# Kernel tuning notes

Measured on AMD Instinct MI355X. Metric: run time of the kernel, lower is better.

## Reference

```python
import jax, jax.numpy as jnp
import numpy as np

K = 20
EPS = 1e-5


def knn_idx(x, k):
    # x: (B,C,N); returns indices of k nearest neighbors (largest negative sq dist)
    xx = jnp.sum(x * x, axis=1)                       # (B,N)
    inner = jnp.einsum('bcn,bcm->bnm', x, x)          # (B,N,N)
    dist = 2.0 * inner - xx[:, :, None] - xx[:, None, :]
    return jax.lax.top_k(dist, k)[1]                  # (B,N,k)


def gather_nb(x, idx):
    # x: (B,C,N), idx: (B,N,k) -> (B,N,k,C)
    xt = jnp.transpose(x, (0, 2, 1))
    return jax.vmap(lambda t, i: t[i])(xt, idx)


def bn(x, g, b, m, v):
    # eval-mode batchnorm over channel axis 1
    sh = [1] * x.ndim
    sh[1] = -1
    inv = g / jnp.sqrt(v + EPS)
    return (x - m.reshape(sh)) * inv.reshape(sh) + b.reshape(sh)


def graph_feature(x, k=K):
    # x: (B,C,N) -> (B,3C,N,k): [neighbor, center, center-neighbor]
    idx = knn_idx(x, k)
    nb = gather_nb(x, idx)                            # (B,N,k,C)
    ctr = jnp.broadcast_to(jnp.transpose(x, (0, 2, 1))[:, :, None, :], nb.shape)
    f = jnp.concatenate([nb, ctr, ctr - nb], axis=-1)
    return jnp.transpose(f, (0, 3, 1, 2))


def att_pool(x, g, b, m, v, W, wb):
    # x: (B,C,N,k); BN->ReLU->1x1 conv -> softmax over k -> weighted sum
    h = jax.nn.relu(bn(x, g, b, m, v))
    act = jnp.einsum('bcnk,oc->bonk', h, W) + wb[None, :, None, None]
    scores = jax.nn.softmax(act, axis=-1)
    return jnp.sum(x * scores, axis=-1)               # (B,C,N)


def lafe(x, W1, b1, W2, b2, W3, b3):
    # local attention extraction; x: (B,3,N) -> (B,16,N)
    idx = knn_idx(x, K)
    nb = gather_nb(x, idx)                            # (B,N,k,3)
    ctr = jnp.broadcast_to(jnp.transpose(x, (0, 2, 1))[:, :, None, :], nb.shape)
    x_n = ctr - nb
    new_f = jnp.einsum('bnkc,oc->bnko', ctr, W1) + b1
    self_att = jnp.einsum('bnko,o->bnk', new_f, W3[0]) + b3[0]
    edge = jnp.einsum('bnkc,oc->bnko', x_n, W2) + b2  # (B,N,k,16)
    nb_att = jnp.einsum('bnko,o->bnk', edge, W3[0]) + b3[0]
    logits = self_att + nb_att                        # (B,N,k)
    coefs = jax.nn.softmax(jax.nn.leaky_relu(logits, 0.01), axis=-1)
    vals = jnp.einsum('bnk,bnko->bno', coefs, edge)   # (B,N,16)
    return jnp.transpose(jax.nn.elu(vals), (0, 2, 1))


def _forward(x, law1, lab1, law2, lab2, law3, lab3,
             mlp_w, mlp_b, mlp_g, mlp_be, mlp_m, mlp_v,
             c1_w, bn1_g, bn1_b, bn1_m, bn1_v,
             p1_g, p1_b, p1_m, p1_v, p1_w, p1_wb,
             c2_w, bn2_g, bn2_b, bn2_m, bn2_v,
             p2_g, p2_b, p2_m, p2_v, p2_w, p2_wb,
             c3_w, bn3_g, bn3_b, bn3_m, bn3_v):
    xm = lafe(x, law1, lab1, law2, lab2, law3, lab3)          # (B,16,N)
    x_manet = jnp.concatenate([x, xm], axis=1)                # (B,19,N)
    x_mlp = jax.nn.relu(bn(jnp.einsum('bcn,oc->bon', x_manet, mlp_w) + mlp_b[None, :, None],
                           mlp_g, mlp_be, mlp_m, mlp_v))      # (B,256,N)
    g = graph_feature(x_manet)                                # (B,57,N,k)
    h1 = jax.nn.leaky_relu(bn(jnp.einsum('bcnk,oc->bonk', g, c1_w),
                              bn1_g, bn1_b, bn1_m, bn1_v), 0.2)
    x_p1 = att_pool(h1, p1_g, p1_b, p1_m, p1_v, p1_w, p1_wb)  # (B,64,N)
    x_c1 = jnp.concatenate([x_manet, x_p1], axis=1)           # (B,83,N)
    g2 = graph_feature(x_c1)                                  # (B,249,N,k)
    h2 = jax.nn.leaky_relu(bn(jnp.einsum('bcnk,oc->bonk', g2, c2_w),
                              bn2_g, bn2_b, bn2_m, bn2_v), 0.2)
    x_p2 = att_pool(h2, p2_g, p2_b, p2_m, p2_v, p2_w, p2_wb)  # (B,256,N)
    x_c2 = jnp.concatenate([x_mlp, x_p2], axis=1)             # (B,512,N)
    return jax.nn.leaky_relu(bn(jnp.einsum('bcn,oc->bon', x_c2, c3_w),
                                bn3_g, bn3_b, bn3_m, bn3_v), 0.2)


def setup_inputs() -> dict:
    key = jax.random.key(0)
    ks = iter(jax.random.split(key, 16))
    f32 = jnp.float32
    def W(*s):
        return jax.random.normal(next(ks), s, f32) * 0.05
    B, N = 8, 2048
    def bn_params(c):
        return jnp.ones((c,), f32), jnp.zeros((c,), f32), jnp.zeros((c,), f32), jnp.ones((c,), f32)
    d = {}
    d['x'] = jax.random.normal(next(ks), (B, 3, N), f32)
    d['law1'], d['lab1'] = W(16, 3), jnp.zeros((16,), f32)
    d['law2'], d['lab2'] = W(16, 3), jnp.zeros((16,), f32)
    d['law3'], d['lab3'] = W(1, 16), jnp.zeros((1,), f32)
    d['mlp_w'], d['mlp_b'] = W(256, 19), jnp.zeros((256,), f32)
    d['mlp_g'], d['mlp_be'], d['mlp_m'], d['mlp_v'] = bn_params(256)
    d['c1_w'] = W(64, 57)
    d['bn1_g'], d['bn1_b'], d['bn1_m'], d['bn1_v'] = bn_params(64)
    d['p1_g'], d['p1_b'], d['p1_m'], d['p1_v'] = bn_params(64)
    d['p1_w'], d['p1_wb'] = W(64, 64), jnp.zeros((64,), f32)
    d['c2_w'] = W(256, 249)
    d['bn2_g'], d['bn2_b'], d['bn2_m'], d['bn2_v'] = bn_params(256)
    d['p2_g'], d['p2_b'], d['p2_m'], d['p2_v'] = bn_params(256)
    d['p2_w'], d['p2_wb'] = W(256, 256), jnp.zeros((256,), f32)
    d['c3_w'] = W(512, 512)
    d['bn3_g'], d['bn3_b'], d['bn3_m'], d['bn3_v'] = bn_params(512)
    return d


def reference(x, law1, lab1, law2, lab2, law3, lab3,
              mlp_w, mlp_b, mlp_g, mlp_be, mlp_m, mlp_v,
              c1_w, bn1_g, bn1_b, bn1_m, bn1_v,
              p1_g, p1_b, p1_m, p1_v, p1_w, p1_wb,
              c2_w, bn2_g, bn2_b, bn2_m, bn2_v,
              p2_g, p2_b, p2_m, p2_v, p2_w, p2_wb,
              c3_w, bn3_g, bn3_b, bn3_m, bn3_v):
    return _forward(x, law1, lab1, law2, lab2, law3, lab3,
                    mlp_w, mlp_b, mlp_g, mlp_be, mlp_m, mlp_v,
                    c1_w, bn1_g, bn1_b, bn1_m, bn1_v,
                    p1_g, p1_b, p1_m, p1_v, p1_w, p1_wb,
                    c2_w, bn2_g, bn2_b, bn2_m, bn2_v,
                    p2_g, p2_b, p2_m, p2_v, p2_w, p2_wb,
                    c3_w, bn3_g, bn3_b, bn3_m, bn3_v)
```

## Files before the change

kernel.cpp:

```cpp
#include <hip/hip_runtime.h>
#include <math.h>
#include <float.h>

#define NB 8
#define NP 2048
#define KNN 20
#define BN_EPS 1e-5f

typedef __attribute__((ext_vector_type(8))) short short8v;
typedef __attribute__((ext_vector_type(4))) float f32x4;
typedef __attribute__((ext_vector_type(16))) float f32x16;

__device__ __forceinline__ float leakyf(float x, float s) { return x >= 0.f ? x : s * x; }

__device__ __forceinline__ unsigned short f2bf(float f) {
  unsigned u = __float_as_uint(f);
  u = u + 0x7fffu + ((u >> 16) & 1u);
  return (unsigned short)(u >> 16);
}
__device__ __forceinline__ float bf2f(unsigned short h) {
  return __uint_as_float((unsigned)h << 16);
}
__device__ __forceinline__ unsigned sortkey(float f) {
  unsigned u = __float_as_uint(f);
  return (u & 0x80000000u) ? ~u : (u | 0x80000000u);
}

__global__ void transpose_k(const float* __restrict__ src, float* __restrict__ dst, int O, int C) {
  int i = blockIdx.x * 256 + threadIdx.x;
  if (i < O * C) { int o = i / C, c = i - o * C; dst[c * O + o] = src[i]; }
}

__global__ void copy_ch_k(const float* __restrict__ src, int srcC,
                          float* __restrict__ dst, int dstC, int row0, int nch) {
  int i = blockIdx.x * 256 + threadIdx.x;
  int total = NB * nch * NP;
  if (i < total) {
    int n = i & (NP - 1); int t = i >> 11; int c = t % nch; int b = t / nch;
    dst[((size_t)b * dstC + row0 + c) * NP + n] = src[((size_t)b * srcC + c) * NP + n];
  }
}

__global__ void xx_k(const float* __restrict__ src, int C, float* __restrict__ xx) {
  int i = blockIdx.x * 256 + threadIdx.x;
  if (i < NB * NP) {
    int n = i & (NP - 1); int b = i >> 11;
    const float* xb = src + (size_t)b * C * NP + n;
    float s = 0.f;
    for (int c = 0; c < C; ++c) { float v = xb[(size_t)c * NP]; s += v * v; }
    xx[i] = s;
  }
}

#define DKC 16
__global__ __launch_bounds__(256) void dist_k(const float* __restrict__ src, int C,
                                              const float* __restrict__ xx,
                                              float* __restrict__ D, int b0) {
  __shared__ float sA[DKC][64];
  __shared__ float sB[DKC][64];
  int bz = blockIdx.z; int b = b0 + bz;
  int n0 = blockIdx.x * 64, m0 = blockIdx.y * 64;
  int tid = threadIdx.x;
  int tn = tid >> 4, tm = tid & 15;
  float acc[4][4] = {};
  const float* xb = src + (size_t)b * C * NP;
  for (int k0 = 0; k0 < C; k0 += DKC) {
    for (int t = tid; t < DKC * 64; t += 256) {
      int kk = t >> 6, i = t & 63;
      int c = k0 + kk;
      float a = 0.f, bb = 0.f;
      if (c < C) { a = xb[(size_t)c * NP + n0 + i]; bb = xb[(size_t)c * NP + m0 + i]; }
      sA[kk][i] = a; sB[kk][i] = bb;
    }
    __syncthreads();
#pragma unroll
    for (int kk = 0; kk < DKC; ++kk) {
      float av[4], bv[4];
#pragma unroll
      for (int q = 0; q < 4; ++q) { av[q] = sA[kk][tn * 4 + q]; bv[q] = sB[kk][tm * 4 + q]; }
#pragma unroll
      for (int qi = 0; qi < 4; ++qi)
#pragma unroll
        for (int qj = 0; qj < 4; ++qj) acc[qi][qj] += av[qi] * bv[qj];
    }
    __syncthreads();
  }
  const float* xxb = xx + (size_t)b * NP;
#pragma unroll
  for (int qi = 0; qi < 4; ++qi) {
    int n = n0 + tn * 4 + qi; float xn = xxb[n];
#pragma unroll
    for (int qj = 0; qj < 4; ++qj) {
      int m = m0 + tm * 4 + qj;
      D[((size_t)bz * NP + n) * NP + m] = 2.f * acc[qi][qj] - xn - xxb[m];
    }
  }
}

__global__ __launch_bounds__(64) void topk_k(const float* __restrict__ D,
                                             int* __restrict__ idxo, int rowbase) {
  int row = blockIdx.x;
  const float* d = D + (size_t)row * NP;
  int lane = threadIdx.x;
  float v[32];
#pragma unroll
  for (int j = 0; j < 32; ++j) v[j] = d[lane + 64 * j];
  int* out = idxo + (size_t)(rowbase + row) * KNN;
  for (int it = 0; it < KNN; ++it) {
    float bv = v[0]; int bj = 0;
#pragma unroll
    for (int j = 1; j < 32; ++j) { if (v[j] > bv) { bv = v[j]; bj = j; } }
    int bm = lane + 64 * bj;
    unsigned long long key = ((unsigned long long)sortkey(bv) << 32) | (unsigned)(~bm);
#pragma unroll
    for (int off = 1; off < 64; off <<= 1) {
      unsigned long long ok = __shfl_xor(key, off);
      if (ok > key) key = ok;
    }
    int bmw = ~(unsigned)key;
    if (lane == 0) out[it] = bmw;
    if ((bmw & 63) == lane) v[bmw >> 6] = -FLT_MAX;
  }
}

__global__ __launch_bounds__(64) void lafe_k(const float* __restrict__ x, const int* __restrict__ idx,
                                             const float* __restrict__ W1, const float* __restrict__ b1,
                                             const float* __restrict__ W2, const float* __restrict__ b2,
                                             const float* __restrict__ W3, const float* __restrict__ b3,
                                             float* __restrict__ x_manet) {
  int t = blockIdx.x * 64 + threadIdx.x;
  if (t >= NB * NP) return;
  int b = t >> 11, n = t & (NP - 1);
  const float* xb = x + (size_t)b * 3 * NP;
  float ctr[3];
#pragma unroll
  for (int c = 0; c < 3; ++c) ctr[c] = xb[c * NP + n];
  float self_s = b3[0];
#pragma unroll
  for (int o = 0; o < 16; ++o) {
    float nf = b1[o];
#pragma unroll
    for (int c = 0; c < 3; ++c) nf += ctr[c] * W1[o * 3 + c];
    self_s += nf * W3[o];
  }
  const int* id = idx + (size_t)t * KNN;
  float logit[KNN];
  float mx = -FLT_MAX;
  for (int k = 0; k < KNN; ++k) {
    int j = id[k];
    float xn[3];
#pragma unroll
    for (int c = 0; c < 3; ++c) xn[c] = ctr[c] - xb[c * NP + j];
    float natt = b3[0];
#pragma unroll
    for (int o = 0; o < 16; ++o) {
      float e = b2[o];
#pragma unroll
      for (int c = 0; c < 3; ++c) e += xn[c] * W2[o * 3 + c];
      natt += e * W3[o];
    }
    float lg = self_s + natt;
    lg = leakyf(lg, 0.01f);
    logit[k] = lg; mx = fmaxf(mx, lg);
  }
  float s = 0.f;
#pragma unroll
  for (int k = 0; k < KNN; ++k) { logit[k] = expf(logit[k] - mx); s += logit[k]; }
  float invs = 1.f / s;
  float vals[16] = {};
  for (int k = 0; k < KNN; ++k) {
    int j = id[k];
    float xn[3];
#pragma unroll
    for (int c = 0; c < 3; ++c) xn[c] = ctr[c] - xb[c * NP + j];
    float w = logit[k] * invs;
#pragma unroll
    for (int o = 0; o < 16; ++o) {
      float e = b2[o];
#pragma unroll
      for (int c = 0; c < 3; ++c) e += xn[c] * W2[o * 3 + c];
      vals[o] += w * e;
    }
  }
#pragma unroll
  for (int o = 0; o < 16; ++o) {
    float v = vals[o];
    v = v > 0.f ? v : expm1f(v);
    x_manet[((size_t)b * 19 + 3 + o) * NP + n] = v;
  }
}

__global__ __launch_bounds__(256) void mlp_k(const float* __restrict__ xman, const float* __restrict__ wt,
                                             const float* __restrict__ bias,
                                             const float* __restrict__ g, const float* __restrict__ be,
                                             const float* __restrict__ m, const float* __restrict__ v,
                                             unsigned short* __restrict__ actT) {
  int o0 = (threadIdx.x & 31) * 8;
  int n = blockIdx.x * 8 + (threadIdx.x >> 5);
  int b = blockIdx.z;
  const float* xb = xman + (size_t)b * 19 * NP;
  float acc[8];
#pragma unroll
  for (int q = 0; q < 8; ++q) acc[q] = bias[o0 + q];
  for (int c = 0; c < 19; ++c) {
    float xv = xb[(size_t)c * NP + n];
    const float4* w4 = reinterpret_cast<const float4*>(wt + c * 256 + o0);
    float4 wa = w4[0], wb4 = w4[1];
    float wr[8] = {wa.x, wa.y, wa.z, wa.w, wb4.x, wb4.y, wb4.z, wb4.w};
#pragma unroll
    for (int q = 0; q < 8; ++q) acc[q] += xv * wr[q];
  }
  short8v hi8, lo8;
#pragma unroll
  for (int q = 0; q < 8; ++q) {
    int o = o0 + q;
    float inv = g[o] / sqrtf(v[o] + BN_EPS);
    float z = fmaxf((acc[q] - m[o]) * inv + be[o], 0.f);
    unsigned short h = f2bf(z);
    hi8[q] = (short)h;
    lo8[q] = (short)f2bf(z - bf2f(h));
  }
  size_t base = ((size_t)b * NP + n) * 1024;
  *reinterpret_cast<short8v*>(actT + base + o0) = hi8;
  *reinterpret_cast<short8v*>(actT + base + 512 + o0) = lo8;
}

__global__ __launch_bounds__(64, 1) void conv1pool_k(
    const float* __restrict__ xman, const int* __restrict__ idx,
    const float* __restrict__ c1wt,
    const float* __restrict__ b1g, const float* __restrict__ b1b,
    const float* __restrict__ b1m, const float* __restrict__ b1v,
    const float* __restrict__ p1g, const float* __restrict__ p1b,
    const float* __restrict__ p1m, const float* __restrict__ p1v,
    const float* __restrict__ p1wt, const float* __restrict__ p1wb,
    float* __restrict__ x_c1) {
  __shared__ __align__(16) float sg[64 * 20];
  __shared__ int jid[KNN];
  __shared__ float sctr[19];
  int t = blockIdx.x;
  int b = t >> 11, n = t & (NP - 1);
  int lane = threadIdx.x;
  const float* xb = xman + (size_t)b * 19 * NP;
  if (lane < KNN) jid[lane] = idx[(size_t)t * KNN + lane];
  else if (lane >= 32 && lane < 32 + 19) sctr[lane - 32] = xb[(size_t)(lane - 32) * NP + n];
  __syncthreads();
  for (int e = lane; e < 19 * KNN; e += 64) {
    int c = e / KNN, k = e - c * KNN;
    float ctrv = sctr[c];
    float nbv = xb[(size_t)c * NP + jid[k]];
    sg[c * 20 + k] = nbv;
    sg[(19 + c) * 20 + k] = ctrv;
    sg[(38 + c) * 20 + k] = ctrv - nbv;
  }
  __syncthreads();
  float h[KNN] = {};
  for (int c = 0; c < 57; ++c) {
    float wv = c1wt[c * 64 + lane];
    const float4* gp = reinterpret_cast<const float4*>(sg + c * 20);
    float4 A = gp[0], Bv = gp[1], Cv = gp[2], Dv = gp[3], E = gp[4];
    float gv[20] = {A.x,A.y,A.z,A.w,Bv.x,Bv.y,Bv.z,Bv.w,Cv.x,Cv.y,Cv.z,Cv.w,Dv.x,Dv.y,Dv.z,Dv.w,E.x,E.y,E.z,E.w};
#pragma unroll
    for (int k = 0; k < KNN; ++k) h[k] += wv * gv[k];
  }
  float inv1 = b1g[lane] / sqrtf(b1v[lane] + BN_EPS);
  float m1 = b1m[lane], bb1 = b1b[lane];
  float h1[KNN];
#pragma unroll
  for (int k = 0; k < KNN; ++k) {
    float z = (h[k] - m1) * inv1 + bb1;
    h1[k] = leakyf(z, 0.2f);
  }
  float pinv = p1g[lane] / sqrtf(p1v[lane] + BN_EPS);
  float pm = p1m[lane], pb = p1b[lane];
  __syncthreads();
#pragma unroll
  for (int k = 0; k < KNN; ++k) sg[lane * 20 + k] = fmaxf((h1[k] - pm) * pinv + pb, 0.f);
  __syncthreads();
  float act[KNN] = {};
  for (int c = 0; c < 64; ++c) {
    float wv = p1wt[c * 64 + lane];
    const float4* gp = reinterpret_cast<const float4*>(sg + c * 20);
    float4 A = gp[0], Bv = gp[1], Cv = gp[2], Dv = gp[3], E = gp[4];
    float gv[20] = {A.x,A.y,A.z,A.w,Bv.x,Bv.y,Bv.z,Bv.w,Cv.x,Cv.y,Cv.z,Cv.w,Dv.x,Dv.y,Dv.z,Dv.w,E.x,E.y,E.z,E.w};
#pragma unroll
    for (int k = 0; k < KNN; ++k) act[k] += wv * gv[k];
  }
  float wb = p1wb[lane];
  float mx = -FLT_MAX;
#pragma unroll
  for (int k = 0; k < KNN; ++k) { act[k] += wb; mx = fmaxf(mx, act[k]); }
  float s = 0.f, outv = 0.f;
#pragma unroll
  for (int k = 0; k < KNN; ++k) {
    float e = expf(act[k] - mx);
    s += e; outv += h1[k] * e;
  }
  x_c1[((size_t)b * 83 + 19 + lane) * NP + n] = outv / s;
}

__global__ void prep2_k(const float* __restrict__ c2w, unsigned short* __restrict__ Wnc) {
  int i = blockIdx.x * 256 + threadIdx.x;
  if (i >= 256 * 192) return;
  int o = i / 192, c = i - o * 192;
  unsigned short v = 0;
  if (c < 83) v = f2bf(c2w[o * 249 + c] - c2w[o * 249 + 166 + c]);
  else if (c >= 96 && c < 96 + 83) {
    int cc = c - 96;
    v = f2bf(c2w[o * 249 + 83 + cc] + c2w[o * 249 + 166 + cc]);
  }
  Wnc[o * 192 + c] = v;
}

__global__ void castbf_k(const float* __restrict__ src, unsigned short* __restrict__ dst, int n) {
  int i = blockIdx.x * 256 + threadIdx.x;
  if (i < n) dst[i] = f2bf(src[i]);
}

__global__ void packw_k(const unsigned short* __restrict__ Wsrc, int KS, int Kstride,
                        unsigned short* __restrict__ dst) {
  int i = blockIdx.x * 256 + threadIdx.x;
  if (i >= 8 * KS * 64) return;
  int lane = i & 63;
  int ks = (i >> 6) % KS;
  int ot = i / (64 * KS);
  int o = ot * 32 + (lane & 31);
  int c = ks * 16 + 8 * (lane >> 5);
#pragma unroll
  for (int e = 0; e < 8; ++e) dst[i * 8 + e] = Wsrc[(size_t)o * Kstride + c + e];
}

__global__ void prep3_k(const float* __restrict__ c3w, unsigned short* __restrict__ W3p) {
  int i = blockIdx.x * 256 + threadIdx.x;
  if (i >= 512 * 1024) return;
  int o = i >> 10, k = i & 1023;
  W3p[i] = f2bf(c3w[o * 512 + (k & 511)]);
}

__global__ void prepbn_k(const float* g2, const float* b2, const float* m2, const float* v2,
                         const float* pg, const float* pb, const float* pm, const float* pv,
                         float* __restrict__ fold) {
  int o = threadIdx.x;
  float s2 = g2[o] / sqrtf(v2[o] + BN_EPS);
  fold[o] = s2; fold[256 + o] = b2[o] - m2[o] * s2;
  float sp = pg[o] / sqrtf(pv[o] + BN_EPS);
  fold[512 + o] = sp; fold[768 + o] = pb[o] - pm[o] * sp;
}

__global__ void prepbn3_k(const float* g, const float* bb, const float* m, const float* v,
                          float* __restrict__ fold3) {
  int o = blockIdx.x * 256 + threadIdx.x;
  if (o < 512) {
    float s = g[o] / sqrtf(v[o] + BN_EPS);
    fold3[o] = s;
    fold3[512 + o] = bb[o] - m[o] * s;
  }
}

__global__ __launch_bounds__(256) void t2bf_k(const float* __restrict__ xc1,
                                              unsigned short* __restrict__ xc1T) {
  __shared__ unsigned short tile[256 * 96];
  int b = blockIdx.y;
  int n0 = blockIdx.x * 256;
  int tid = threadIdx.x;
  const float* xb = xc1 + (size_t)b * 83 * NP;
  for (int c = 0; c < 83; ++c)
    tile[tid * 96 + c] = f2bf(xb[(size_t)c * NP + n0 + tid]);
#pragma unroll
  for (int c = 83; c < 96; ++c) tile[tid * 96 + c] = 0;
  __syncthreads();
  const float4* src = (const float4*)tile;
  float4* dst = (float4*)(xc1T + ((size_t)b * NP + n0) * 96);
  for (int i = tid; i < 3072; i += 256) dst[i] = src[i];
}

__global__ __launch_bounds__(256, 2) void conv2mfma_k(
    const unsigned short* __restrict__ xc1T, const int* __restrict__ idx,
    const unsigned short* __restrict__ pw1, const unsigned short* __restrict__ pw2,
    const float* __restrict__ fold, unsigned short* __restrict__ actT) {
  __shared__ unsigned short nbF[2 * 6 * 64 * 8];
  __shared__ unsigned short hhF[2 * 16 * 64 * 8];
  __shared__ int jid[64];
  int tid = threadIdx.x;
  int t0 = blockIdx.x * 2;
  int b = t0 >> 11, n0 = t0 & (NP - 1);

  if (tid < 64) {
    int p = tid >> 5, kk = tid & 31;
    int kc = kk < KNN ? kk : KNN - 1;
    jid[tid] = idx[(size_t)(t0 + p) * KNN + kc];
  }
  __syncthreads();
  for (int it = tid; it < 768; it += 256) {
    int p = it >= 384; int rem = it - p * 384;
    int kk = rem / 12, seg = rem - kk * 12;
    int j = jid[p * 32 + kk];
    short8v v = *reinterpret_cast<const short8v*>(xc1T + ((size_t)b * NP + j) * 96 + seg * 8);
    int ks = seg >> 1, hi = seg & 1;
    *reinterpret_cast<short8v*>(&nbF[(((p * 6 + ks) << 6) + hi * 32 + kk) * 8]) = v;
  }
  __syncthreads();

  int w = tid >> 6, l = tid & 63;
  int kk = l & 31, hi = l >> 5;
  int ot0 = w * 2, ot1 = w * 2 + 1;
  const short8v* pw1v = (const short8v*)pw1;
  const short8v* pw2v = (const short8v*)pw2;

  f32x16 acc[2][2];
#pragma unroll
  for (int p = 0; p < 2; ++p)
#pragma unroll
    for (int nt = 0; nt < 2; ++nt)
#pragma unroll
      for (int r = 0; r < 16; ++r) acc[p][nt][r] = 0.f;

#pragma unroll
  for (int ks = 0; ks < 6; ++ks) {
    short8v b0 = pw1v[(ot0 * 12 + ks) * 64 + l];
    short8v b1 = pw1v[(ot1 * 12 + ks) * 64 + l];
    short8v a0 = *reinterpret_cast<const short8v*>(&nbF[((ks << 6) + l) * 8]);
    short8v a1 = *reinterpret_cast<const short8v*>(&nbF[(((6 + ks) << 6) + l) * 8]);
    acc[0][0] = __builtin_amdgcn_mfma_f32_32x32x16_bf16(a0, b0, acc[0][0], 0, 0, 0);
    acc[0][1] = __builtin_amdgcn_mfma_f32_32x32x16_bf16(a0, b1, acc[0][1], 0, 0, 0);
    acc[1][0] = __builtin_amdgcn_mfma_f32_32x32x16_bf16(a1, b0, acc[1][0], 0, 0, 0);
    acc[1][1] = __builtin_amdgcn_mfma_f32_32x32x16_bf16(a1, b1, acc[1][1], 0, 0, 0);
  }
  const unsigned short* ct0 = xc1T + ((size_t)b * NP + n0) * 96 + 8 * hi;
  const unsigned short* ct1 = ct0 + 96;
#pragma unroll
  for (int ks = 0; ks < 6; ++ks) {
    short8v b0 = pw1v[(ot0 * 12 + 6 + ks) * 64 + l];
    short8v b1 = pw1v[(ot1 * 12 + 6 + ks) * 64 + l];
    short8v a0 = *reinterpret_cast<const short8v*>(ct0 + ks * 16);
    short8v a1 = *reinterpret_cast<const short8v*>(ct1 + ks * 16);
    acc[0][0] = __builtin_amdgcn_mfma_f32_32x32x16_bf16(a0, b0, acc[0][0], 0, 0, 0);
    acc[0][1] = __builtin_amdgcn_mfma_f32_32x32x16_bf16(a0, b1, acc[0][1], 0, 0, 0);
    acc[1][0] = __builtin_amdgcn_mfma_f32_32x32x16_bf16(a1, b0, acc[1][0], 0, 0, 0);
    acc[1][1] = __builtin_amdgcn_mfma_f32_32x32x16_bf16(a1, b1, acc[1][1], 0, 0, 0);
  }

#pragma unroll
  for (int p = 0; p < 2; ++p)
#pragma unroll
    for (int nt = 0; nt < 2; ++nt) {
      int o = w * 64 + nt * 32 + kk;
      float s2 = fold[o], o2 = fold[256 + o];
      float sp = fold[512 + o], op = fold[768 + o];
      int cbase = (p * 16 + (o >> 4)) * 64 + ((o >> 3) & 1) * 32;
#pragma unroll
      for (int r = 0; r < 16; ++r) {
        int row = (r & 3) + 8 * (r >> 2) + 4 * hi;
        float z = leakyf(acc[p][nt][r] * s2 + o2, 0.2f);
        acc[p][nt][r] = z;
        float hh = fmaxf(z * sp + op, 0.f);
        hhF[(cbase + row) * 8 + (o & 7)] = f2bf(hh);
      }
    }
  __syncthreads();

  f32x16 acc2[2][2];
#pragma unroll
  for (int p = 0; p < 2; ++p)
#pragma unroll
    for (int nt = 0; nt < 2; ++nt)
#pragma unroll
      for (int r = 0; r < 16; ++r) acc2[p][nt][r] = 0.f;
#pragma unroll
  for (int ks = 0; ks < 16; ++ks) {
    short8v b0 = pw2v[(ot0 * 16 + ks) * 64 + l];
    short8v b1 = pw2v[(ot1 * 16 + ks) * 64 + l];
    short8v a0 = *reinterpret_cast<const short8v*>(&hhF[((ks << 6) + l) * 8]);
    short8v a1 = *reinterpret_cast<const short8v*>(&hhF[(((16 + ks) << 6) + l) * 8]);
    acc2[0][0] = __builtin_amdgcn_mfma_f32_32x32x16_bf16(a0, b0, acc2[0][0], 0, 0, 0);
    acc2[0][1] = __builtin_amdgcn_mfma_f32_32x32x16_bf16(a0, b1, acc2[0][1], 0, 0, 0);
    acc2[1][0] = __builtin_amdgcn_mfma_f32_32x32x16_bf16(a1, b0, acc2[1][0], 0, 0, 0);
    acc2[1][1] = __builtin_amdgcn_mfma_f32_32x32x16_bf16(a1, b1, acc2[1][1], 0, 0, 0);
  }

#pragma unroll
  for (int p = 0; p < 2; ++p) {
    size_t base = ((size_t)b * NP + n0 + p) * 1024;
#pragma unroll
    for (int nt = 0; nt < 2; ++nt) {
      int o = w * 64 + nt * 32 + kk;
      float mx = -FLT_MAX;
#pragma unroll
      for (int r = 0; r < 16; ++r) {
        int row = (r & 3) + 8 * (r >> 2) + 4 * hi;
        if (row < KNN) mx = fmaxf(mx, acc2[p][nt][r]);
      }
      mx = fmaxf(mx, __shfl_xor(mx, 32));
      float s = 0.f, num = 0.f;
#pragma unroll
      for (int r = 0; r < 16; ++r) {
        int row = (r & 3) + 8 * (r >> 2) + 4 * hi;
        if (row < KNN) {
          float e = __expf(acc2[p][nt][r] - mx);
          s += e; num += e * acc[p][nt][r];
        }
      }
      s += __shfl_xor(s, 32);
      num += __shfl_xor(num, 32);
      if (hi == 0) {
        float z = num / s;
        unsigned short h = f2bf(z);
        actT[base + 256 + o] = h;
        actT[base + 768 + o] = f2bf(z - bf2f(h));
      }
    }
  }
}

__global__ __launch_bounds__(256) void conv3mfma_k(const unsigned short* __restrict__ actT,
                                                   const unsigned short* __restrict__ W3p,
                                                   const float* __restrict__ fold3,
                                                   float* __restrict__ out) {
  __shared__ unsigned short sA[128 * 64];
  __shared__ unsigned short sB[128 * 64];
  int b = blockIdx.z;
  int o0 = blockIdx.x * 128, n0 = blockIdx.y * 128;
  int tid = threadIdx.x;
  int wave = tid >> 6, lane = tid & 63;
  int wr = wave >> 1, wc = wave & 1;
  int lrow = lane & 15, lkb2 = (lane >> 4) * 16, lr4 = (lane >> 4) * 4;

  f32x4 acc[4][4];
#pragma unroll
  for (int mt = 0; mt < 4; ++mt)
#pragma unroll
    for (int nt = 0; nt < 4; ++nt) acc[mt][nt] = (f32x4){0.f, 0.f, 0.f, 0.f};

  for (int k0 = 0; k0 < 1024; k0 += 64) {
    for (int i = tid; i < 2048; i += 256) {
      int half = i >> 10;
      int r = (i >> 3) & 127;
      int ci = i & 7;
      const unsigned short* src = half
          ? (actT + ((size_t)b * NP + n0 + r) * 1024 + k0 + ci * 8)
          : (W3p + (size_t)(o0 + r) * 1024 + k0 + ci * 8);
      short8v vv = *reinterpret_cast<const short8v*>(src);
      int byteoff = (r * 128 + ci * 16) ^ ((r & 7) << 4);
      *reinterpret_cast<short8v*>((char*)(half ? sB : sA) + byteoff) = vv;
    }
    __syncthreads();
#pragma unroll
    for (int ks = 0; ks < 2; ++ks) {
      short8v afr[4], bfr[4];
#pragma unroll
      for (int mt = 0; mt < 4; ++mt) {
        int r = wr * 64 + mt * 16 + lrow;
        afr[mt] = *reinterpret_cast<const short8v*>((char*)sA + ((r * 128 + ks * 64 + lkb2) ^ ((r & 7) << 4)));
      }
#pragma unroll
      for (int nt = 0; nt < 4; ++nt) {
        int r = wc * 64 + nt * 16 + lrow;
        bfr[nt] = *reinterpret_cast<const short8v*>((char*)sB + ((r * 128 + ks * 64 + lkb2) ^ ((r & 7) << 4)));
      }
#pragma unroll
      for (int mt = 0; mt < 4; ++mt)
#pragma unroll
        for (int nt = 0; nt < 4; ++nt)
          acc[mt][nt] = __builtin_amdgcn_mfma_f32_16x16x32_bf16(afr[mt], bfr[nt], acc[mt][nt], 0, 0, 0);
    }
    __syncthreads();
  }
#pragma unroll
  for (int mt = 0; mt < 4; ++mt) {
#pragma unroll
    for (int r = 0; r < 4; ++r) {
      int o = o0 + wr * 64 + mt * 16 + lr4 + r;
      float s3 = fold3[o], b3 = fold3[512 + o];
      float* op = out + ((size_t)b * 512 + o) * NP + n0 + wc * 64 + lrow;
#pragma unroll
      for (int nt = 0; nt < 4; ++nt) {
        float z = acc[mt][nt][r] * s3 + b3;
        op[nt * 16] = leakyf(z, 0.2f);
      }
    }
  }
}

extern "C" void kernel_launch(void* const* d_in, const int* in_sizes, int n_in,
                              void* d_out, int out_size, void* d_ws, size_t ws_size,
                              hipStream_t stream) {
  const float* x     = (const float*)d_in[0];
  const float* law1  = (const float*)d_in[1];
  const float* lab1  = (const float*)d_in[2];
  const float* law2  = (const float*)d_in[3];
  const float* lab2  = (const float*)d_in[4];
  const float* law3  = (const float*)d_in[5];
  const float* lab3  = (const float*)d_in[6];
  const float* mlp_w = (const float*)d_in[7];
  const float* mlp_b = (const float*)d_in[8];
  const float* mlp_g = (const float*)d_in[9];
  const float* mlp_be= (const float*)d_in[10];
  const float* mlp_m = (const float*)d_in[11];
  const float* mlp_v = (const float*)d_in[12];
  const float* c1_w  = (const float*)d_in[13];
  const float* bn1_g = (const float*)d_in[14];
  const float* bn1_b = (const float*)d_in[15];
  const float* bn1_m = (const float*)d_in[16];
  const float* bn1_v = (const float*)d_in[17];
  const float* p1_g  = (const float*)d_in[18];
  const float* p1_b  = (const float*)d_in[19];
  const float* p1_m  = (const float*)d_in[20];
  const float* p1_v  = (const float*)d_in[21];
  const float* p1_w  = (const float*)d_in[22];
  const float* p1_wb = (const float*)d_in[23];
  const float* c2_w  = (const float*)d_in[24];
  const float* bn2_g = (const float*)d_in[25];
  const float* bn2_b = (const float*)d_in[26];
  const float* bn2_m = (const float*)d_in[27];
  const float* bn2_v = (const float*)d_in[28];
  const float* p2_g  = (const float*)d_in[29];
  const float* p2_b  = (const float*)d_in[30];
  const float* p2_m  = (const float*)d_in[31];
  const float* p2_v  = (const float*)d_in[32];
  const float* p2_w  = (const float*)d_in[33];
  const float* p2_wb = (const float*)d_in[34];
  const float* c3_w  = (const float*)d_in[35];
  const float* bn3_g = (const float*)d_in[36];
  const float* bn3_b = (const float*)d_in[37];
  const float* bn3_m = (const float*)d_in[38];
  const float* bn3_v = (const float*)d_in[39];

  char* wsb = (char*)d_ws;
  size_t off = 0;
  auto alloc = [&](size_t elems) -> float* {
    float* p = (float*)(wsb + off);
    off += elems * sizeof(float);
    off = (off + 255) & ~(size_t)255;
    return p;
  };
  float* c1_wt  = alloc(57 * 64);
  float* mlp_wt = alloc(19 * 256);
  float* p1_wt  = alloc(64 * 64);
  unsigned short* Wnc = (unsigned short*)alloc(256 * 192 / 2);
  unsigned short* p2wB = (unsigned short*)alloc(256 * 256 / 2);
  unsigned short* pw1 = (unsigned short*)alloc(8 * 12 * 64 * 8 / 2);
  unsigned short* pw2 = (unsigned short*)alloc(8 * 16 * 64 * 8 / 2);
  unsigned short* W3p  = (unsigned short*)alloc((size_t)512 * 1024 / 2);
  float* fold2  = alloc(1024);
  float* fold3  = alloc(1024);
  float* xxbuf  = alloc((size_t)NB * NP);
  float* x_manet= alloc((size_t)NB * 19 * NP);
  float* x_c1   = alloc((size_t)NB * 83 * NP);
  unsigned short* xc1T = (unsigned short*)alloc((size_t)NB * NP * 96 / 2);
  unsigned short* actT = (unsigned short*)alloc((size_t)NB * NP * 1024 / 2);
  int*   idxbuf = (int*)alloc((size_t)NB * NP * KNN);
  float* Dbuf   = (float*)(wsb + off);
  size_t fullD = (size_t)NB * NP * NP * sizeof(float);
  int nbc = (off + fullD <= ws_size) ? NB : 1;

  transpose_k<<<(64 * 57 + 255) / 256, 256, 0, stream>>>(c1_w, c1_wt, 64, 57);
  transpose_k<<<(256 * 19 + 255) / 256, 256, 0, stream>>>(mlp_w, mlp_wt, 256, 19);
  transpose_k<<<(64 * 64 + 255) / 256, 256, 0, stream>>>(p1_w, p1_wt, 64, 64);
  prep2_k<<<192, 256, 0, stream>>>(c2_w, Wnc);
  castbf_k<<<256, 256, 0, stream>>>(p2_w, p2wB, 256 * 256);
  packw_k<<<24, 256, 0, stream>>>(Wnc, 12, 192, pw1);
  packw_k<<<32, 256, 0, stream>>>(p2wB, 16, 256, pw2);
  prep3_k<<<2048, 256, 0, stream>>>(c3_w, W3p);
  prepbn_k<<<1, 256, 0, stream>>>(bn2_g, bn2_b, bn2_m, bn2_v, p2_g, p2_b, p2_m, p2_v, fold2);
  prepbn3_k<<<2, 256, 0, stream>>>(bn3_g, bn3_b, bn3_m, bn3_v, fold3);

  auto knn = [&](const float* src, int C) {
    xx_k<<<(NB * NP + 255) / 256, 256, 0, stream>>>(src, C, xxbuf);
    for (int b0 = 0; b0 < NB; b0 += nbc) {
      dist_k<<<dim3(NP / 64, NP / 64, nbc), 256, 0, stream>>>(src, C, xxbuf, Dbuf, b0);
      topk_k<<<nbc * NP, 64, 0, stream>>>(Dbuf, idxbuf, b0 * NP);
    }
  };

  copy_ch_k<<<(NB * 3 * NP + 255) / 256, 256, 0, stream>>>(x, 3, x_manet, 19, 0, 3);

  knn(x, 3);
  lafe_k<<<(NB * NP) / 64, 64, 0, stream>>>(x, idxbuf, law1, lab1, law2, lab2, law3, lab3, x_manet);

  mlp_k<<<dim3(NP / 8, 1, NB), 256, 0, stream>>>(x_manet, mlp_wt, mlp_b, mlp_g, mlp_be, mlp_m, mlp_v, actT);

  knn(x_manet, 19);
  conv1pool_k<<<NB * NP, 64, 0, stream>>>(x_manet, idxbuf, c1_wt,
                                          bn1_g, bn1_b, bn1_m, bn1_v,
                                          p1_g, p1_b, p1_m, p1_v,
                                          p1_wt, p1_wb, x_c1);
  copy_ch_k<<<(NB * 19 * NP + 255) / 256, 256, 0, stream>>>(x_manet, 19, x_c1, 83, 0, 19);

  knn(x_c1, 83);
  t2bf_k<<<dim3(NP / 256, NB), 256, 0, stream>>>(x_c1, xc1T);
  conv2mfma_k<<<NB * NP / 2, 256, 0, stream>>>(xc1T, idxbuf, pw1, pw2, fold2, actT);

  conv3mfma_k<<<dim3(512 / 128, NP / 128, NB), 256, 0, stream>>>(actT, W3p, fold3,
                                                                 (float*)d_out);
}
```

Measured before the change: 918.5 us.

## Fold conv1 center term algebraically, merge prep kernels, swizzle conv2 LDS

```diff
diff --git a/kernel.cpp b/kernel.cpp
--- a/kernel.cpp
+++ b/kernel.cpp
@@ -24,11 +24,6 @@
 __device__ __forceinline__ unsigned sortkey(float f) {
   unsigned u = __float_as_uint(f);
   return (u & 0x80000000u) ? ~u : (u | 0x80000000u);
-}
-
-__global__ void transpose_k(const float* __restrict__ src, float* __restrict__ dst, int O, int C) {
-  int i = blockIdx.x * 256 + threadIdx.x;
-  if (i < O * C) { int o = i / C, c = i - o * C; dst[c * O + o] = src[i]; }
 }
 
 __global__ void copy_ch_k(const float* __restrict__ src, int srcC,
@@ -49,6 +44,96 @@
     float s = 0.f;
     for (int c = 0; c < C; ++c) { float v = xb[(size_t)c * NP]; s += v * v; }
     xx[i] = s;
+  }
+}
+
+__global__ void prepall_k(const float* __restrict__ c1w, const float* __restrict__ mlpw,
+                          const float* __restrict__ p1w, const float* __restrict__ c2w,
+                          const float* __restrict__ p2w, const float* __restrict__ c3w,
+                          const float* g2, const float* b2, const float* m2, const float* v2,
+                          const float* pg, const float* pb, const float* pm, const float* pv,
+                          const float* g3, const float* b3, const float* m3, const float* v3,
+                          float* __restrict__ wn1t, float* __restrict__ wc1t,
+                          float* __restrict__ mlp_wt, float* __restrict__ p1_wt,
+                          unsigned short* __restrict__ Wnc, unsigned short* __restrict__ p2wB,
+                          unsigned short* __restrict__ W3p,
+                          float* __restrict__ fold2, float* __restrict__ fold3) {
+  int i = blockIdx.x * 256 + threadIdx.x;
+  if (i < 19 * 64) {
+    int c = i >> 6, o = i & 63;
+    float wd = c1w[o * 57 + 38 + c];
+    wn1t[i] = c1w[o * 57 + c] - wd;
+    wc1t[i] = c1w[o * 57 + 19 + c] + wd;
+    return;
+  }
+  i -= 19 * 64;
+  if (i < 19 * 256) {
+    int o = i / 19, c = i - o * 19;
+    mlp_wt[c * 256 + o] = mlpw[i];
+    return;
+  }
+  i -= 19 * 256;
+  if (i < 64 * 64) {
+    int o = i >> 6, c = i & 63;
+    p1_wt[c * 64 + o] = p1w[i];
+    return;
+  }
+  i -= 64 * 64;
+  if (i < 256 * 192) {
+    int o = i / 192, c = i - o * 192;
+    unsigned short v = 0;
+    if (c < 83) v = f2bf(c2w[o * 249 + c] - c2w[o * 249 + 166 + c]);
+    else if (c >= 96 && c < 96 + 83) {
+      int cc = c - 96;
+      v = f2bf(c2w[o * 249 + 83 + cc] + c2w[o * 249 + 166 + cc]);
+    }
+    Wnc[i] = v;
+    return;
+  }
+  i -= 256 * 192;
+  if (i < 256 * 256) { p2wB[i] = f2bf(p2w[i]); return; }
+  i -= 256 * 256;
+  if (i < 512 * 1024) {
+    int o = i >> 10, k = i & 1023;
+    W3p[i] = f2bf(c3w[o * 512 + (k & 511)]);
+    return;
+  }
+  i -= 512 * 1024;
+  if (i < 256) {
+    int o = i;
+    float s2 = g2[o] / sqrtf(v2[o] + BN_EPS);
+    fold2[o] = s2; fold2[256 + o] = b2[o] - m2[o] * s2;
+    float sp = pg[o] / sqrtf(pv[o] + BN_EPS);
+    fold2[512 + o] = sp; fold2[768 + o] = pb[o] - pm[o] * sp;
+    return;
+  }
+  i -= 256;
+  if (i < 512) {
+    int o = i;
+    float s = g3[o] / sqrtf(v3[o] + BN_EPS);
+    fold3[o] = s;
+    fold3[512 + o] = b3[o] - m3[o] * s;
+  }
+}
+#define PREPALL_TOTAL (19*64 + 19*256 + 64*64 + 256*192 + 256*256 + 512*1024 + 256 + 512)
+
+__global__ void packall_k(const unsigned short* __restrict__ Wnc,
+                          const unsigned short* __restrict__ p2wB,
+                          unsigned short* __restrict__ pw1, unsigned short* __restrict__ pw2) {
+  int i = blockIdx.x * 256 + threadIdx.x;
+  if (i < 8 * 12 * 64) {
+    int lane = i & 63, ks = (i >> 6) % 12, ot = i / (64 * 12);
+    int o = ot * 32 + (lane & 31), c = ks * 16 + 8 * (lane >> 5);
+#pragma unroll
+    for (int e = 0; e < 8; ++e) pw1[i * 8 + e] = Wnc[(size_t)o * 192 + c + e];
+    return;
+  }
+  int j = i - 8 * 12 * 64;
+  if (j < 8 * 16 * 64) {
+    int lane = j & 63, ks = (j >> 6) % 16, ot = j / (64 * 16);
+    int o = ot * 32 + (lane & 31), c = ks * 16 + 8 * (lane >> 5);
+#pragma unroll
+    for (int e = 0; e < 8; ++e) pw2[j * 8 + e] = p2wB[(size_t)o * 256 + c + e];
   }
 }
 
@@ -225,9 +310,21 @@
   *reinterpret_cast<short8v*>(actT + base + 512 + o0) = lo8;
 }
 
+__global__ __launch_bounds__(256) void hctr1_k(const float* __restrict__ xman,
+                                               const float* __restrict__ wc1t,
+                                               float* __restrict__ hctr1) {
+  int o = threadIdx.x;
+  int n = blockIdx.x * 4 + threadIdx.y;
+  int b = blockIdx.z;
+  const float* xb = xman + (size_t)b * 19 * NP + n;
+  float acc = 0.f;
+  for (int c = 0; c < 19; ++c) acc += wc1t[c * 64 + o] * xb[(size_t)c * NP];
+  hctr1[((size_t)b * 64 + o) * NP + n] = acc;
+}
+
 __global__ __launch_bounds__(64, 1) void conv1pool_k(
     const float* __restrict__ xman, const int* __restrict__ idx,
-    const float* __restrict__ c1wt,
+    const float* __restrict__ wn1t, const float* __restrict__ hctr1,
     const float* __restrict__ b1g, const float* __restrict__ b1b,
     const float* __restrict__ b1m, const float* __restrict__ b1v,
     const float* __restrict__ p1g, const float* __restrict__ p1b,
@@ -236,26 +333,23 @@
     float* __restrict__ x_c1) {
   __shared__ __align__(16) float sg[64 * 20];
   __shared__ int jid[KNN];
-  __shared__ float sctr[19];
   int t = blockIdx.x;
   int b = t >> 11, n = t & (NP - 1);
   int lane = threadIdx.x;
   const float* xb = xman + (size_t)b * 19 * NP;
   if (lane < KNN) jid[lane] = idx[(size_t)t * KNN + lane];
-  else if (lane >= 32 && lane < 32 + 19) sctr[lane - 32] = xb[(size_t)(lane - 32) * NP + n];
   __syncthreads();
   for (int e = lane; e < 19 * KNN; e += 64) {
     int c = e / KNN, k = e - c * KNN;
-    float ctrv = sctr[c];
-    float nbv = xb[(size_t)c * NP + jid[k]];
-    sg[c * 20 + k] = nbv;
-    sg[(19 + c) * 20 + k] = ctrv;
-    sg[(38 + c) * 20 + k] = ctrv - nbv;
+    sg[c * 20 + k] = xb[(size_t)c * NP + jid[k]];
   }
   __syncthreads();
-  float h[KNN] = {};
-  for (int c = 0; c < 57; ++c) {
-    float wv = c1wt[c * 64 + lane];
+  float hc = hctr1[((size_t)b * 64 + lane) * NP + n];
+  float h[KNN];
+#pragma unroll
+  for (int k = 0; k < KNN; ++k) h[k] = hc;
+  for (int c = 0; c < 19; ++c) {
+    float wv = wn1t[c * 64 + lane];
     const float4* gp = reinterpret_cast<const float4*>(sg + c * 20);
     float4 A = gp[0], Bv = gp[1], Cv = gp[2], Dv = gp[3], E = gp[4];
     float gv[20] = {A.x,A.y,A.z,A.w,Bv.x,Bv.y,Bv.z,Bv.w,Cv.x,Cv.y,Cv.z,Cv.w,Dv.x,Dv.y,Dv.z,Dv.w,E.x,E.y,E.z,E.w};
@@ -296,64 +390,6 @@
     s += e; outv += h1[k] * e;
   }
   x_c1[((size_t)b * 83 + 19 + lane) * NP + n] = outv / s;
-}
-
-__global__ void prep2_k(const float* __restrict__ c2w, unsigned short* __restrict__ Wnc) {
-  int i = blockIdx.x * 256 + threadIdx.x;
-  if (i >= 256 * 192) return;
-  int o = i / 192, c = i - o * 192;
-  unsigned short v = 0;
-  if (c < 83) v = f2bf(c2w[o * 249 + c] - c2w[o * 249 + 166 + c]);
-  else if (c >= 96 && c < 96 + 83) {
-    int cc = c - 96;
-    v = f2bf(c2w[o * 249 + 83 + cc] + c2w[o * 249 + 166 + cc]);
-  }
-  Wnc[o * 192 + c] = v;
-}
-
-__global__ void castbf_k(const float* __restrict__ src, unsigned short* __restrict__ dst, int n) {
-  int i = blockIdx.x * 256 + threadIdx.x;
-  if (i < n) dst[i] = f2bf(src[i]);
-}
-
-__global__ void packw_k(const unsigned short* __restrict__ Wsrc, int KS, int Kstride,
-                        unsigned short* __restrict__ dst) {
-  int i = blockIdx.x * 256 + threadIdx.x;
-  if (i >= 8 * KS * 64) return;
-  int lane = i & 63;
-  int ks = (i >> 6) % KS;
-  int ot = i / (64 * KS);
-  int o = ot * 32 + (lane & 31);
-  int c = ks * 16 + 8 * (lane >> 5);
-#pragma unroll
-  for (int e = 0; e < 8; ++e) dst[i * 8 + e] = Wsrc[(size_t)o * Kstride + c + e];
-}
-
-__global__ void prep3_k(const float* __restrict__ c3w, unsigned short* __restrict__ W3p) {
-  int i = blockIdx.x * 256 + threadIdx.x;
-  if (i >= 512 * 1024) return;
-  int o = i >> 10, k = i & 1023;
-  W3p[i] = f2bf(c3w[o * 512 + (k & 511)]);
-}
-
-__global__ void prepbn_k(const float* g2, const float* b2, const float* m2, const float* v2,
-                         const float* pg, const float* pb, const float* pm, const float* pv,
-                         float* __restrict__ fold) {
-  int o = threadIdx.x;
-  float s2 = g2[o] / sqrtf(v2[o] + BN_EPS);
-  fold[o] = s2; fold[256 + o] = b2[o] - m2[o] * s2;
-  float sp = pg[o] / sqrtf(pv[o] + BN_EPS);
-  fold[512 + o] = sp; fold[768 + o] = pb[o] - pm[o] * sp;
-}
-
-__global__ void prepbn3_k(const float* g, const float* bb, const float* m, const float* v,
-                          float* __restrict__ fold3) {
-  int o = blockIdx.x * 256 + threadIdx.x;
-  if (o < 512) {
-    float s = g[o] / sqrtf(v[o] + BN_EPS);
-    fold3[o] = s;
-    fold3[512 + o] = bb[o] - m[o] * s;
-  }
 }
 
 __global__ __launch_bounds__(256) void t2bf_k(const float* __restrict__ xc1,
@@ -447,13 +483,14 @@
       float s2 = fold[o], o2 = fold[256 + o];
       float sp = fold[512 + o], op = fold[768 + o];
       int cbase = (p * 16 + (o >> 4)) * 64 + ((o >> 3) & 1) * 32;
+      int s = (o >> 3) & 3;
 #pragma unroll
       for (int r = 0; r < 16; ++r) {
         int row = (r & 3) + 8 * (r >> 2) + 4 * hi;
         float z = leakyf(acc[p][nt][r] * s2 + o2, 0.2f);
         acc[p][nt][r] = z;
         float hh = fmaxf(z * sp + op, 0.f);
-        hhF[(cbase + row) * 8 + (o & 7)] = f2bf(hh);
+        hhF[((cbase + row) ^ s) * 8 + (o & 7)] = f2bf(hh);
       }
     }
   __syncthreads();
@@ -467,10 +504,11 @@
       for (int r = 0; r < 16; ++r) acc2[p][nt][r] = 0.f;
 #pragma unroll
   for (int ks = 0; ks < 16; ++ks) {
+    int sr = (l >> 5) | ((ks & 1) << 1);
     short8v b0 = pw2v[(ot0 * 16 + ks) * 64 + l];
     short8v b1 = pw2v[(ot1 * 16 + ks) * 64 + l];
-    short8v a0 = *reinterpret_cast<const short8v*>(&hhF[((ks << 6) + l) * 8]);
-    short8v a1 = *reinterpret_cast<const short8v*>(&hhF[(((16 + ks) << 6) + l) * 8]);
+    short8v a0 = *reinterpret_cast<const short8v*>(&hhF[((((ks << 6) + l)) ^ sr) * 8]);
+    short8v a1 = *reinterpret_cast<const short8v*>(&hhF[(((((16 + ks) << 6) + l)) ^ sr) * 8]);
     acc2[0][0] = __builtin_amdgcn_mfma_f32_32x32x16_bf16(a0, b0, acc2[0][0], 0, 0, 0);
     acc2[0][1] = __builtin_amdgcn_mfma_f32_32x32x16_bf16(a0, b1, acc2[0][1], 0, 0, 0);
     acc2[1][0] = __builtin_amdgcn_mfma_f32_32x32x16_bf16(a1, b0, acc2[1][0], 0, 0, 0);
@@ -632,7 +670,8 @@
     off = (off + 255) & ~(size_t)255;
     return p;
   };
-  float* c1_wt  = alloc(57 * 64);
+  float* wn1t   = alloc(19 * 64);
+  float* wc1t   = alloc(19 * 64);
   float* mlp_wt = alloc(19 * 256);
   float* p1_wt  = alloc(64 * 64);
   unsigned short* Wnc = (unsigned short*)alloc(256 * 192 / 2);
@@ -645,6 +684,7 @@
   float* xxbuf  = alloc((size_t)NB * NP);
   float* x_manet= alloc((size_t)NB * 19 * NP);
   float* x_c1   = alloc((size_t)NB * 83 * NP);
+  float* hctr1  = alloc((size_t)NB * 64 * NP);
   unsigned short* xc1T = (unsigned short*)alloc((size_t)NB * NP * 96 / 2);
   unsigned short* actT = (unsigned short*)alloc((size_t)NB * NP * 1024 / 2);
   int*   idxbuf = (int*)alloc((size_t)NB * NP * KNN);
@@ -652,16 +692,12 @@
   size_t fullD = (size_t)NB * NP * NP * sizeof(float);
   int nbc = (off + fullD <= ws_size) ? NB : 1;
 
-  transpose_k<<<(64 * 57 + 255) / 256, 256, 0, stream>>>(c1_w, c1_wt, 64, 57);
-  transpose_k<<<(256 * 19 + 255) / 256, 256, 0, stream>>>(mlp_w, mlp_wt, 256, 19);
-  transpose_k<<<(64 * 64 + 255) / 256, 256, 0, stream>>>(p1_w, p1_wt, 64, 64);
-  prep2_k<<<192, 256, 0, stream>>>(c2_w, Wnc);
-  castbf_k<<<256, 256, 0, stream>>>(p2_w, p2wB, 256 * 256);
-  packw_k<<<24, 256, 0, stream>>>(Wnc, 12, 192, pw1);
-  packw_k<<<32, 256, 0, stream>>>(p2wB, 16, 256, pw2);
-  prep3_k<<<2048, 256, 0, stream>>>(c3_w, W3p);
-  prepbn_k<<<1, 256, 0, stream>>>(bn2_g, bn2_b, bn2_m, bn2_v, p2_g, p2_b, p2_m, p2_v, fold2);
-  prepbn3_k<<<2, 256, 0, stream>>>(bn3_g, bn3_b, bn3_m, bn3_v, fold3);
+  prepall_k<<<(PREPALL_TOTAL + 255) / 256, 256, 0, stream>>>(
+      c1_w, mlp_w, p1_w, c2_w, p2_w, c3_w,
+      bn2_g, bn2_b, bn2_m, bn2_v, p2_g, p2_b, p2_m, p2_v,
+      bn3_g, bn3_b, bn3_m, bn3_v,
+      wn1t, wc1t, mlp_wt, p1_wt, Wnc, p2wB, W3p, fold2, fold3);
+  packall_k<<<56, 256, 0, stream>>>(Wnc, p2wB, pw1, pw2);
 
   auto knn = [&](const float* src, int C) {
     xx_k<<<(NB * NP + 255) / 256, 256, 0, stream>>>(src, C, xxbuf);
@@ -679,7 +715,8 @@
   mlp_k<<<dim3(NP / 8, 1, NB), 256, 0, stream>>>(x_manet, mlp_wt, mlp_b, mlp_g, mlp_be, mlp_m, mlp_v, actT);
 
   knn(x_manet, 19);
-  conv1pool_k<<<NB * NP, 64, 0, stream>>>(x_manet, idxbuf, c1_wt,
+  hctr1_k<<<dim3(NP / 4, 1, NB), dim3(64, 4), 0, stream>>>(x_manet, wc1t, hctr1);
+  conv1pool_k<<<NB * NP, 64, 0, stream>>>(x_manet, idxbuf, wn1t, hctr1,
                                           bn1_g, bn1_b, bn1_m, bn1_v,
                                           p1_g, p1_b, p1_m, p1_v,
                                           p1_wt, p1_wb, x_c1);
```

Measured after the change: 898.7 us. 2.1% less time.
